# Optimization experiments

Measured on AMD Instinct MI355X. Metric: run time of the kernel, lower is better.

The kernel has to match this reference:

```python
import jax, jax.numpy as jnp
import numpy as np

H = 16      # num_head
D = 1024    # feat_dim
DK = D // H # per-head dim
B, S = 2, 2048


def setup_inputs() -> dict:
    key = jax.random.key(0)
    ks = jax.random.split(key, 11)
    scale = 1.0 / np.sqrt(D)
    inp = {
        'query': jax.random.normal(ks[0], (B, S, D), jnp.float32),
        'key':   jax.random.normal(ks[1], (B, S, D), jnp.float32),
        'value': jax.random.normal(ks[2], (B, S, D), jnp.float32),
        # causal lower-triangular mask (seq, seq); 0 entries get -1e9
        'mask':  jnp.tril(jnp.ones((S, S), jnp.int32)),
        # torch nn.Linear params: y = x @ W.T + b
        'w_q': jax.random.normal(ks[3], (D, D), jnp.float32) * scale,
        'b_q': jax.random.normal(ks[4], (D,), jnp.float32) * scale,
        'w_k': jax.random.normal(ks[5], (D, D), jnp.float32) * scale,
        'b_k': jax.random.normal(ks[6], (D,), jnp.float32) * scale,
        'w_v': jax.random.normal(ks[7], (D, D), jnp.float32) * scale,
        'b_v': jax.random.normal(ks[8], (D,), jnp.float32) * scale,
        'w_out': jax.random.normal(ks[9], (D, D), jnp.float32) * scale,
        'b_out': jax.random.normal(ks[10], (D,), jnp.float32) * scale,
    }
    return inp


def reference(query, key, value, mask, w_q, b_q, w_k, b_k, w_v, b_v, w_out, b_out):
    b = query.shape[0]
    # projections + split heads -> (b, h, s, d_k)
    def proj(x, w, bias):
        y = x @ w.T + bias
        return y.reshape(b, -1, H, DK).transpose(0, 2, 1, 3)
    q = proj(query, w_q, b_q)
    k = proj(key, w_k, b_k)
    v = proj(value, w_v, b_v)
    # scaled dot-product attention with materialized score matrix
    scores = jnp.einsum('bhqd,bhkd->bhqk', q, k) / np.sqrt(DK).astype(jnp.float32)
    scores = jnp.where(mask == 0, jnp.float32(-1e9), scores)
    attn = jax.nn.softmax(scores, axis=-1)  # dropout is identity in eval mode
    x = jnp.einsum('bhqk,bhkd->bhqd', attn, v)
    x = x.transpose(0, 2, 1, 3).reshape(b, -1, H * DK)
    return x @ w_out.T + b_out
```

## Files before the change

kernel.cpp:

```cpp
#include <hip/hip_runtime.h>

typedef unsigned short u16;
typedef __attribute__((ext_vector_type(8))) short short8;
typedef __attribute__((ext_vector_type(8))) unsigned short u16x8;
typedef __attribute__((ext_vector_type(4))) float floatx4;
typedef __attribute__((ext_vector_type(16))) float floatx16;

#define S2LOG 0.18033688f

__device__ __forceinline__ u16 f2bf(float f) {
    unsigned int u = __float_as_uint(f);
    return (u16)((u + 0x7FFFu + ((u >> 16) & 1u)) >> 16);
}
__device__ __forceinline__ void gl_lds16(const u16* g, u16* l) {
    __builtin_amdgcn_global_load_lds(
        (const __attribute__((address_space(1))) void*)g,
        (__attribute__((address_space(3))) void*)l, 16, 0, 0);
}

__global__ __launch_bounds__(256) void cvt_all(
    const float* __restrict__ q, const float* __restrict__ k, const float* __restrict__ v,
    const float* __restrict__ wq, const float* __restrict__ wk,
    const float* __restrict__ wv, const float* __restrict__ wo,
    u16* __restrict__ ws)
{
    const int b = blockIdx.x, t = threadIdx.x;
    const float* src; u16* dst; long blk;
    if      (b < 2048) { src = q;  dst = ws;            blk = b; }
    else if (b < 4096) { src = k;  dst = ws + 4194304;  blk = b - 2048; }
    else if (b < 6144) { src = v;  dst = ws + 8388608;  blk = b - 4096; }
    else if (b < 6656) { src = wq; dst = ws + 12582912; blk = b - 6144; }
    else if (b < 7168) { src = wk; dst = ws + 13631488; blk = b - 6656; }
    else if (b < 7680) { src = wv; dst = ws + 14680064; blk = b - 7168; }
    else               { src = wo; dst = ws + 15728640; blk = b - 7680; }
    const long i = blk * 2048 + (long)t * 8;
    const float4 a = *(const float4*)(src + i);
    const float4 c = *(const float4*)(src + i + 4);
    u16x8 o;
    o[0] = f2bf(a.x); o[1] = f2bf(a.y); o[2] = f2bf(a.z); o[3] = f2bf(a.w);
    o[4] = f2bf(c.x); o[5] = f2bf(c.y); o[6] = f2bf(c.z); o[7] = f2bf(c.w);
    *(u16x8*)(dst + i) = o;
}

__device__ __forceinline__ void gemm_core64(
    const u16* __restrict__ A, const u16* __restrict__ Bw,
    int m0, int n0, floatx4 (&acc)[2][4])
{
    __shared__ u16 As[3][128 * 32];
    __shared__ u16 Bs[3][64 * 32];
    const int t = threadIdx.x, w = t >> 6;
    const int lane = t & 63, col = lane & 15, quad = lane >> 4;
    const int swz = quad ^ (col & 3) ^ ((col >> 2) & 3);

#pragma unroll
    for (int i = 0; i < 2; ++i)
#pragma unroll
        for (int j = 0; j < 4; ++j) acc[i][j] = (floatx4)0.f;

    auto stage = [&](int k0, int buf) {
#pragma unroll
        for (int jj = 0; jj < 2; ++jj) {
            const int c = jj * 256 + t;
            const int row = c >> 2;
            const int kc = (c & 3) ^ (row & 3) ^ ((row >> 2) & 3);
            gl_lds16(A + (size_t)(m0 + row) * 1024 + k0 + kc * 8,
                     As[buf] + (jj * 256 + w * 64) * 8);
        }
        {
            const int row = t >> 2;
            const int kc = (t & 3) ^ (row & 3) ^ ((row >> 2) & 3);
            gl_lds16(Bw + (size_t)(n0 + row) * 1024 + k0 + kc * 8,
                     Bs[buf] + (w * 64) * 8);
        }
    };

    stage(0, 0);
    stage(32, 1);
    int cur = 0, nxt = 2;
    for (int k0 = 0; k0 < 1024; k0 += 32) {
        if (k0 + 32 < 1024) asm volatile("s_waitcnt vmcnt(3)" ::: "memory");
        else                asm volatile("s_waitcnt vmcnt(0)" ::: "memory");
        __builtin_amdgcn_s_barrier();
        if (k0 + 64 < 1024) stage(k0 + 64, nxt);
        short8 af[2], bf[4];
#pragma unroll
        for (int i = 0; i < 2; ++i)
            af[i] = *(const short8*)&As[cur][((w * 32 + i * 16 + col) * 4 + swz) * 8];
#pragma unroll
        for (int j = 0; j < 4; ++j)
            bf[j] = *(const short8*)&Bs[cur][((j * 16 + col) * 4 + swz) * 8];
        __builtin_amdgcn_s_setprio(1);
#pragma unroll
        for (int i = 0; i < 2; ++i)
#pragma unroll
            for (int j = 0; j < 4; ++j)
                acc[i][j] = __builtin_amdgcn_mfma_f32_16x16x32_bf16(
                    af[i], bf[j], acc[i][j], 0, 0, 0);
        __builtin_amdgcn_s_setprio(0);
        asm volatile("s_waitcnt lgkmcnt(0)" ::: "memory");
        cur = (cur == 2) ? 0 : cur + 1;
        nxt = (nxt == 2) ? 0 : nxt + 1;
    }
}

__device__ __forceinline__ void gemm_core128(
    const u16* __restrict__ A, const u16* __restrict__ Bw,
    int m0, int n0, floatx4 (&acc)[4][4])
{
    __shared__ u16 As[3][128 * 32];
    __shared__ u16 Bs[3][128 * 32];
    const int t = threadIdx.x, w = t >> 6;
    const int lane = t & 63, col = lane & 15, quad = lane >> 4;
    const int wr = (w >> 1) * 64, wc = (w & 1) * 64;
    const int swz = quad ^ (col & 3) ^ ((col >> 2) & 3);

#pragma unroll
    for (int i = 0; i < 4; ++i)
#pragma unroll
        for (int j = 0; j < 4; ++j) acc[i][j] = (floatx4)0.f;

    auto stage = [&](int k0, int buf) {
#pragma unroll
        for (int jj = 0; jj < 2; ++jj) {
            const int c = jj * 256 + t;
            const int row = c >> 2;
            const int kc = (c & 3) ^ (row & 3) ^ ((row >> 2) & 3);
            gl_lds16(A + (size_t)(m0 + row) * 1024 + k0 + kc * 8,
                     As[buf] + (jj * 256 + w * 64) * 8);
            gl_lds16(Bw + (size_t)(n0 + row) * 1024 + k0 + kc * 8,
                     Bs[buf] + (jj * 256 + w * 64) * 8);
        }
    };

    stage(0, 0);
    stage(32, 1);
    int cur = 0, nxt = 2;
    for (int k0 = 0; k0 < 1024; k0 += 32) {
        if (k0 + 32 < 1024) asm volatile("s_waitcnt vmcnt(4)" ::: "memory");
        else                asm volatile("s_waitcnt vmcnt(0)" ::: "memory");
        __builtin_amdgcn_s_barrier();
        if (k0 + 64 < 1024) stage(k0 + 64, nxt);
        short8 af[4], bf[4];
#pragma unroll
        for (int i = 0; i < 4; ++i)
            af[i] = *(const short8*)&As[cur][((wr + i * 16 + col) * 4 + swz) * 8];
#pragma unroll
        for (int j = 0; j < 4; ++j)
            bf[j] = *(const short8*)&Bs[cur][((wc + j * 16 + col) * 4 + swz) * 8];
        __builtin_amdgcn_s_setprio(1);
#pragma unroll
        for (int i = 0; i < 4; ++i)
#pragma unroll
            for (int j = 0; j < 4; ++j)
                acc[i][j] = __builtin_amdgcn_mfma_f32_16x16x32_bf16(
                    af[i], bf[j], acc[i][j], 0, 0, 0);
        __builtin_amdgcn_s_setprio(0);
        asm volatile("s_waitcnt lgkmcnt(0)" ::: "memory");
        cur = (cur == 2) ? 0 : cur + 1;
        nxt = (nxt == 2) ? 0 : nxt + 1;
    }
}

__global__ __launch_bounds__(256) void gemm_qkv(
    const u16* __restrict__ xq, const u16* __restrict__ xk, const u16* __restrict__ xv,
    const u16* __restrict__ wqb, const u16* __restrict__ wkb, const u16* __restrict__ wvb,
    const float* __restrict__ bq, const float* __restrict__ bk, const float* __restrict__ bv,
    u16* __restrict__ Qh, u16* __restrict__ Kh, u16* __restrict__ Vt)
{
    const int z = blockIdx.z;
    const u16*   A    = z == 0 ? xq  : z == 1 ? xk  : xv;
    const u16*   Bw   = z == 0 ? wqb : z == 1 ? wkb : wvb;
    const float* bias = z == 0 ? bq  : z == 1 ? bk  : bv;
    u16*         out  = z == 0 ? Qh  : z == 1 ? Kh  : Vt;
    const float  scale = z == 0 ? S2LOG : 1.0f;
    const int m0 = blockIdx.x * 128, n0 = blockIdx.y * 128;

    floatx4 acc[4][4];
    gemm_core128(A, Bw, m0, n0, acc);

    const int t = threadIdx.x, w = t >> 6;
    const int lane = t & 63, col = lane & 15, quad = lane >> 4;
    const int wr = (w >> 1) * 64, wc = (w & 1) * 64;
#pragma unroll
    for (int i = 0; i < 4; ++i)
#pragma unroll
        for (int j = 0; j < 4; ++j)
#pragma unroll
            for (int reg = 0; reg < 4; ++reg) {
                const int gm = m0 + wr + i * 16 + quad * 4 + reg;
                const int gn = n0 + wc + j * 16 + col;
                const float val = (acc[i][j][reg] + bias[gn]) * scale;
                const int bb = gm >> 11, ss = gm & 2047, hh = gn >> 6, dd = gn & 63;
                if (z != 2)
                    out[(((size_t)bb * 16 + hh) * 2048 + ss) * 64 + dd] = f2bf(val);
                else
                    out[(((size_t)bb * 16 + hh) * 64 + dd) * 2048 + ss] = f2bf(val);
            }
}

__global__ __launch_bounds__(256) void gemm_out(
    const u16* __restrict__ A, const u16* __restrict__ Bw,
    const float* __restrict__ bias, float* __restrict__ out)
{
    const int m0 = blockIdx.x * 128, n0 = blockIdx.y * 64;
    floatx4 acc[2][4];
    gemm_core64(A, Bw, m0, n0, acc);
    const int t = threadIdx.x, w = t >> 6;
    const int lane = t & 63, col = lane & 15, quad = lane >> 4;
#pragma unroll
    for (int i = 0; i < 2; ++i)
#pragma unroll
        for (int j = 0; j < 4; ++j)
#pragma unroll
            for (int reg = 0; reg < 4; ++reg) {
                const int gm = m0 + w * 32 + i * 16 + quad * 4 + reg;
                const int gn = n0 + j * 16 + col;
                out[(size_t)gm * 1024 + gn] = acc[i][j][reg] + bias[gn];
            }
}

__global__ __launch_bounds__(512) void attn_mfma(
    const u16* __restrict__ Qh, const u16* __restrict__ Kh,
    const u16* __restrict__ Vt, u16* __restrict__ ctx)
{
    __shared__ u16 lds[40960];
    const int t = threadIdx.x, w = t >> 6;
    const int g = w >> 2, wg = w & 3;
    const int lane = t & 63;
    const int col = lane & 31;
    const int hi  = lane >> 5;
    const int bh = blockIdx.y;
    const int qt = (bh < 16) ? (15 - (int)blockIdx.x) : (int)blockIdx.x;
    const int q0 = qt * 128;
    const u16* qg = Qh + ((size_t)bh * 2048 + q0) * 64;
    const u16* kg = Kh + (size_t)bh * 2048 * 64;
    const u16* vg = Vt + (size_t)bh * 2048 * 64;

    u16* Qs = lds;
    u16* Kg = lds + 8192 + g * 16384;
    u16* Vg = Kg + 8192;

    auto stage = [&](int tile, int buf) {
#pragma unroll
        for (int jj = 0; jj < 2; ++jj) {
            const int cidx = jj * 4 + wg;
            gl_lds16(kg + (size_t)(tile * 64 + jj * 32 + col) * 64 + wg * 16 + hi * 8,
                     Kg + buf * 4096 + cidx * 512);
            gl_lds16(vg + (size_t)(jj * 32 + col) * 2048 + tile * 64 + wg * 16 + hi * 8,
                     Vg + buf * 4096 + cidx * 512);
        }
    };

#pragma unroll
    for (int jj = 0; jj < 2; ++jj) {
        const int cidx = jj * 8 + w;
        gl_lds16(qg + (size_t)((cidx >> 2) * 32 + col) * 64 + (cidx & 3) * 16 + hi * 8,
                 Qs + cidx * 512);
    }
    stage(g, 0);
    asm volatile("s_waitcnt vmcnt(4)" ::: "memory");
    __builtin_amdgcn_s_barrier();

    short8 qf[4];
#pragma unroll
    for (int tq = 0; tq < 4; ++tq)
        qf[tq] = *(const short8*)&Qs[(wg * 4 + tq) * 512 + lane * 8];

    floatx16 oacc[2];
    oacc[0] = (floatx16)0.f; oacc[1] = (floatx16)0.f;
    float ls = 0.f;
    const int qrow = q0 + wg * 32 + col;

    int cur = 0;
    for (int i = 0; i <= qt; ++i) {
        const int kt = 2 * i + g;
        asm volatile("s_waitcnt vmcnt(0)" ::: "memory");
        __builtin_amdgcn_s_barrier();
        if (i + 1 <= qt) stage(2 * (i + 1) + g, cur ^ 1);
        const bool pm = (i == qt);

#pragma unroll
        for (int sub = 0; sub < 2; ++sub) {
            short8 kf[4];
#pragma unroll
            for (int tq = 0; tq < 4; ++tq)
                kf[tq] = *(const short8*)&Kg[cur * 4096 + (sub * 4 + tq) * 512 + lane * 8];

            floatx16 sacc = (floatx16)0.f;
#pragma unroll
            for (int tq = 0; tq < 4; ++tq)
                sacc = __builtin_amdgcn_mfma_f32_32x32x16_bf16(
                    kf[tq], qf[tq], sacc, 0, 0, 0);

            float pe[16];
#pragma unroll
            for (int r = 0; r < 16; ++r)
                pe[r] = __builtin_amdgcn_exp2f(sacc[r]);
            if (pm) {
                const int kbase = kt * 64 + sub * 32;
#pragma unroll
                for (int r = 0; r < 16; ++r) {
                    const int rkv = (r & 3) + 8 * (r >> 2) + 4 * hi;
                    if (kbase + rkv > qrow) pe[r] = 0.f;
                }
            }
#pragma unroll
            for (int r = 0; r < 16; ++r) ls += pe[r];

            short8 pa[2];
#pragma unroll
            for (int s = 0; s < 2; ++s) {
                unsigned A0, A1, B0, B1;
                asm("v_cvt_pk_bf16_f32 %0, %1, %2" : "=v"(A0) : "v"(pe[8*s+0]), "v"(pe[8*s+1]));
                asm("v_cvt_pk_bf16_f32 %0, %1, %2" : "=v"(A1) : "v"(pe[8*s+2]), "v"(pe[8*s+3]));
                asm("v_cvt_pk_bf16_f32 %0, %1, %2" : "=v"(B0) : "v"(pe[8*s+4]), "v"(pe[8*s+5]));
                asm("v_cvt_pk_bf16_f32 %0, %1, %2" : "=v"(B1) : "v"(pe[8*s+6]), "v"(pe[8*s+7]));
                asm("v_permlane32_swap_b32 %0, %1" : "+v"(A0), "+v"(B0));
                asm("v_permlane32_swap_b32 %0, %1" : "+v"(A1), "+v"(B1));
                union { unsigned u[4]; short8 s8; } cv;
                cv.u[0] = A0; cv.u[1] = A1; cv.u[2] = B0; cv.u[3] = B1;
                pa[s] = cv.s8;
            }

#pragma unroll
            for (int dt = 0; dt < 2; ++dt)
#pragma unroll
                for (int s = 0; s < 2; ++s) {
                    short8 vf = *(const short8*)
                        &Vg[cur * 4096 + (dt * 4 + sub * 2 + s) * 512 + lane * 8];
                    oacc[dt] = __builtin_amdgcn_mfma_f32_32x32x16_bf16(
                        pa[s], vf, oacc[dt], 0, 0, 0);
                }
        }
        cur ^= 1;
    }

    asm volatile("s_waitcnt lgkmcnt(0)" ::: "memory");
    __builtin_amdgcn_s_barrier();

    float* Ob = (float*)(lds + 24576);
    float* Lb = (float*)lds;
    const int slot = wg * 64 + lane;
    if (g == 1) {
#pragma unroll
        for (int r = 0; r < 16; ++r) {
            Ob[slot * 32 + ((r + lane) & 31)]        = oacc[0][r];
            Ob[slot * 32 + ((16 + r + lane) & 31)]   = oacc[1][r];
        }
        Lb[slot] = ls;
    }
    asm volatile("s_waitcnt lgkmcnt(0)" ::: "memory");
    __builtin_amdgcn_s_barrier();
    if (g == 0) {
#pragma unroll
        for (int r = 0; r < 16; ++r) {
            oacc[0][r] += Ob[slot * 32 + ((r + lane) & 31)];
            oacc[1][r] += Ob[slot * 32 + ((16 + r + lane) & 31)];
        }
        ls += Lb[slot];

        const float lt = ls + __shfl_xor(ls, 32);
        const int bb = bh >> 4, hh = bh & 15;
#pragma unroll
        for (int reg = 0; reg < 16; ++reg) {
            const int qr = (reg & 3) + 8 * (reg >> 2) + 4 * hi;
            const float lq = __shfl(lt, qr, 64);
            const float inv = __builtin_amdgcn_rcpf(lq);
            const int qrs = q0 + wg * 32 + qr;
#pragma unroll
            for (int dt = 0; dt < 2; ++dt)
                ctx[((size_t)bb * 2048 + qrs) * 1024 + hh * 64 + dt * 32 + col] =
                    f2bf(oacc[dt][reg] * inv);
        }
    }
}

extern "C" void kernel_launch(void* const* d_in, const int* in_sizes, int n_in,
                              void* d_out, int out_size, void* d_ws, size_t ws_size,
                              hipStream_t stream)
{
    const float* query = (const float*)d_in[0];
    const float* key   = (const float*)d_in[1];
    const float* value = (const float*)d_in[2];
    const float* w_q   = (const float*)d_in[4];
    const float* b_q   = (const float*)d_in[5];
    const float* w_k   = (const float*)d_in[6];
    const float* b_k   = (const float*)d_in[7];
    const float* w_v   = (const float*)d_in[8];
    const float* b_v   = (const float*)d_in[9];
    const float* w_out = (const float*)d_in[10];
    const float* b_out = (const float*)d_in[11];

    u16* W = (u16*)d_ws;
    u16* xq  = W;
    u16* xk  = W + 4194304;
    u16* xv  = W + 8388608;
    u16* wqb = W + 12582912;
    u16* wkb = W + 13631488;
    u16* wvb = W + 14680064;
    u16* wob = W + 15728640;
    u16* Qh  = W + 16777216;
    u16* Kh  = W + 20971520;
    u16* Vtw = W + 25165824;
    u16* ctx = W + 29360128;

    hipLaunchKernelGGL(cvt_all, dim3(8192), dim3(256), 0, stream,
                       query, key, value, w_q, w_k, w_v, w_out, W);

    hipLaunchKernelGGL(gemm_qkv, dim3(32, 8, 3), dim3(256), 0, stream,
                       xq, xk, xv, wqb, wkb, wvb, b_q, b_k, b_v, Qh, Kh, Vtw);

    hipLaunchKernelGGL(attn_mfma, dim3(16, 32), dim3(512), 0, stream, Qh, Kh, Vtw, ctx);

    hipLaunchKernelGGL(gemm_out, dim3(32, 16), dim3(256), 0, stream,
                       ctx, wob, b_out, (float*)d_out);
}
```

Measured before the change: 216.6 us.

## Transpose V epilogue through LDS and split attention output merge across groups

```diff
diff --git a/kernel.cpp b/kernel.cpp
--- a/kernel.cpp
+++ b/kernel.cpp
@@ -89,14 +89,12 @@
 #pragma unroll
         for (int j = 0; j < 4; ++j)
             bf[j] = *(const short8*)&Bs[cur][((j * 16 + col) * 4 + swz) * 8];
-        __builtin_amdgcn_s_setprio(1);
 #pragma unroll
         for (int i = 0; i < 2; ++i)
 #pragma unroll
             for (int j = 0; j < 4; ++j)
                 acc[i][j] = __builtin_amdgcn_mfma_f32_16x16x32_bf16(
                     af[i], bf[j], acc[i][j], 0, 0, 0);
-        __builtin_amdgcn_s_setprio(0);
         asm volatile("s_waitcnt lgkmcnt(0)" ::: "memory");
         cur = (cur == 2) ? 0 : cur + 1;
         nxt = (nxt == 2) ? 0 : nxt + 1;
@@ -105,10 +103,10 @@
 
 __device__ __forceinline__ void gemm_core128(
     const u16* __restrict__ A, const u16* __restrict__ Bw,
-    int m0, int n0, floatx4 (&acc)[4][4])
-{
-    __shared__ u16 As[3][128 * 32];
-    __shared__ u16 Bs[3][128 * 32];
+    int m0, int n0, floatx4 (&acc)[4][4], u16* smem)
+{
+    u16* As = smem;
+    u16* Bs = smem + 12288;
     const int t = threadIdx.x, w = t >> 6;
     const int lane = t & 63, col = lane & 15, quad = lane >> 4;
     const int wr = (w >> 1) * 64, wc = (w & 1) * 64;
@@ -126,9 +124,9 @@
             const int row = c >> 2;
             const int kc = (c & 3) ^ (row & 3) ^ ((row >> 2) & 3);
             gl_lds16(A + (size_t)(m0 + row) * 1024 + k0 + kc * 8,
-                     As[buf] + (jj * 256 + w * 64) * 8);
+                     As + buf * 4096 + (jj * 256 + w * 64) * 8);
             gl_lds16(Bw + (size_t)(n0 + row) * 1024 + k0 + kc * 8,
-                     Bs[buf] + (jj * 256 + w * 64) * 8);
+                     Bs + buf * 4096 + (jj * 256 + w * 64) * 8);
         }
     };
 
@@ -143,18 +141,16 @@
         short8 af[4], bf[4];
 #pragma unroll
         for (int i = 0; i < 4; ++i)
-            af[i] = *(const short8*)&As[cur][((wr + i * 16 + col) * 4 + swz) * 8];
+            af[i] = *(const short8*)&As[cur * 4096 + ((wr + i * 16 + col) * 4 + swz) * 8];
 #pragma unroll
         for (int j = 0; j < 4; ++j)
-            bf[j] = *(const short8*)&Bs[cur][((wc + j * 16 + col) * 4 + swz) * 8];
-        __builtin_amdgcn_s_setprio(1);
+            bf[j] = *(const short8*)&Bs[cur * 4096 + ((wc + j * 16 + col) * 4 + swz) * 8];
 #pragma unroll
         for (int i = 0; i < 4; ++i)
 #pragma unroll
             for (int j = 0; j < 4; ++j)
                 acc[i][j] = __builtin_amdgcn_mfma_f32_16x16x32_bf16(
                     af[i], bf[j], acc[i][j], 0, 0, 0);
-        __builtin_amdgcn_s_setprio(0);
         asm volatile("s_waitcnt lgkmcnt(0)" ::: "memory");
         cur = (cur == 2) ? 0 : cur + 1;
         nxt = (nxt == 2) ? 0 : nxt + 1;
@@ -167,6 +163,7 @@
     const float* __restrict__ bq, const float* __restrict__ bk, const float* __restrict__ bv,
     u16* __restrict__ Qh, u16* __restrict__ Kh, u16* __restrict__ Vt)
 {
+    __shared__ u16 smem[24576];
     const int z = blockIdx.z;
     const u16*   A    = z == 0 ? xq  : z == 1 ? xk  : xv;
     const u16*   Bw   = z == 0 ? wqb : z == 1 ? wkb : wvb;
@@ -176,26 +173,50 @@
     const int m0 = blockIdx.x * 128, n0 = blockIdx.y * 128;
 
     floatx4 acc[4][4];
-    gemm_core128(A, Bw, m0, n0, acc);
+    gemm_core128(A, Bw, m0, n0, acc, smem);
 
     const int t = threadIdx.x, w = t >> 6;
     const int lane = t & 63, col = lane & 15, quad = lane >> 4;
     const int wr = (w >> 1) * 64, wc = (w & 1) * 64;
-#pragma unroll
-    for (int i = 0; i < 4; ++i)
-#pragma unroll
-        for (int j = 0; j < 4; ++j)
-#pragma unroll
-            for (int reg = 0; reg < 4; ++reg) {
-                const int gm = m0 + wr + i * 16 + quad * 4 + reg;
-                const int gn = n0 + wc + j * 16 + col;
-                const float val = (acc[i][j][reg] + bias[gn]) * scale;
-                const int bb = gm >> 11, ss = gm & 2047, hh = gn >> 6, dd = gn & 63;
-                if (z != 2)
+
+    if (z == 2) {
+        __syncthreads();
+#pragma unroll
+        for (int i = 0; i < 4; ++i)
+#pragma unroll
+            for (int j = 0; j < 4; ++j)
+#pragma unroll
+                for (int reg = 0; reg < 4; ++reg) {
+                    const int ssl = wr + i * 16 + quad * 4 + reg;
+                    const int gnl = wc + j * 16 + col;
+                    smem[gnl * 128 + (ssl ^ ((gnl & 7) << 4))] =
+                        f2bf(acc[i][j][reg] + bias[n0 + gnl]);
+                }
+        __syncthreads();
+        const int bb = m0 >> 11, sb = m0 & 2047;
+#pragma unroll
+        for (int c2 = 0; c2 < 8; ++c2) {
+            const int chunk = c2 * 256 + t;
+            const int rg = chunk >> 4, k = chunk & 15;
+            short8 v8 = *(const short8*)&smem[rg * 128 + ((k * 8) ^ ((rg & 7) << 4))];
+            const int gn = n0 + rg;
+            *(short8*)&out[(((size_t)bb * 16 + (gn >> 6)) * 64 + (gn & 63)) * 2048
+                           + sb + k * 8] = v8;
+        }
+    } else {
+#pragma unroll
+        for (int i = 0; i < 4; ++i)
+#pragma unroll
+            for (int j = 0; j < 4; ++j)
+#pragma unroll
+                for (int reg = 0; reg < 4; ++reg) {
+                    const int gm = m0 + wr + i * 16 + quad * 4 + reg;
+                    const int gn = n0 + wc + j * 16 + col;
+                    const float val = (acc[i][j][reg] + bias[gn]) * scale;
+                    const int bb = gm >> 11, ss = gm & 2047, hh = gn >> 6, dd = gn & 63;
                     out[(((size_t)bb * 16 + hh) * 2048 + ss) * 64 + dd] = f2bf(val);
-                else
-                    out[(((size_t)bb * 16 + hh) * 64 + dd) * 2048 + ss] = f2bf(val);
-            }
+                }
+    }
 }
 
 __global__ __launch_bounds__(256) void gemm_out(
@@ -338,40 +359,40 @@
     asm volatile("s_waitcnt lgkmcnt(0)" ::: "memory");
     __builtin_amdgcn_s_barrier();
 
-    float* Ob = (float*)(lds + 24576);
-    float* Lb = (float*)lds;
+    float* Ob0 = (float*)(lds + 24576);
+    float* Ob1 = (float*)(lds + 32768);
+    float* Lb  = (float*)lds;
     const int slot = wg * 64 + lane;
     if (g == 1) {
 #pragma unroll
-        for (int r = 0; r < 16; ++r) {
-            Ob[slot * 32 + ((r + lane) & 31)]        = oacc[0][r];
-            Ob[slot * 32 + ((16 + r + lane) & 31)]   = oacc[1][r];
-        }
+        for (int r = 0; r < 16; ++r)
+            Ob0[slot * 16 + ((r + lane) & 15)] = oacc[0][r];
         Lb[slot] = ls;
+    } else {
+#pragma unroll
+        for (int r = 0; r < 16; ++r)
+            Ob1[slot * 16 + ((r + lane) & 15)] = oacc[1][r];
+        Lb[256 + slot] = ls;
     }
     asm volatile("s_waitcnt lgkmcnt(0)" ::: "memory");
     __builtin_amdgcn_s_barrier();
-    if (g == 0) {
-#pragma unroll
-        for (int r = 0; r < 16; ++r) {
-            oacc[0][r] += Ob[slot * 32 + ((r + lane) & 31)];
-            oacc[1][r] += Ob[slot * 32 + ((16 + r + lane) & 31)];
-        }
-        ls += Lb[slot];
-
-        const float lt = ls + __shfl_xor(ls, 32);
-        const int bb = bh >> 4, hh = bh & 15;
-#pragma unroll
-        for (int reg = 0; reg < 16; ++reg) {
-            const int qr = (reg & 3) + 8 * (reg >> 2) + 4 * hi;
-            const float lq = __shfl(lt, qr, 64);
-            const float inv = __builtin_amdgcn_rcpf(lq);
-            const int qrs = q0 + wg * 32 + qr;
-#pragma unroll
-            for (int dt = 0; dt < 2; ++dt)
-                ctx[((size_t)bb * 2048 + qrs) * 1024 + hh * 64 + dt * 32 + col] =
-                    f2bf(oacc[dt][reg] * inv);
-        }
+
+    const float lsT = ls + Lb[(g == 0 ? 0 : 256) + slot];
+    const float lt = lsT + __shfl_xor(lsT, 32);
+    const int bb = bh >> 4, hh = bh & 15;
+    const int dt = g;
+    float* Obr = (g == 0) ? Ob0 : Ob1;
+#pragma unroll
+    for (int r = 0; r < 16; ++r)
+        oacc[dt][r] += Obr[slot * 16 + ((r + lane) & 15)];
+#pragma unroll
+    for (int reg = 0; reg < 16; ++reg) {
+        const int qr = (reg & 3) + 8 * (reg >> 2) + 4 * hi;
+        const float lq = __shfl(lt, qr, 64);
+        const float inv = __builtin_amdgcn_rcpf(lq);
+        const int qrs = q0 + wg * 32 + qr;
+        ctx[((size_t)bb * 2048 + qrs) * 1024 + hh * 64 + dt * 32 + col] =
+            f2bf(oacc[dt][reg] * inv);
     }
 }
 
```

New measurement: 385.9 us. +78.2%, slower.
